# Performance work log

Measured on AMD Instinct MI355X. Metric: run time of the kernel, lower is better.

## Reference

```python
import jax, jax.numpy as jnp
import numpy as np

C = 768
NH = 8
S_SP = 9            # spatial size per axis; seq = 9**3 = 729
HID = (C * 4 * 2) // 3  # 2048, floor(768*8/3)
E = 3               # num_experts
TOPK = 2
EPS = 1e-5


def setup_inputs() -> dict:
    key = jax.random.key(0)
    ks = jax.random.split(key, 10)
    b = 8
    p = lambda k, shape: (jax.random.normal(k, shape, dtype=jnp.float32) * 0.02)
    return {
        "x": jax.random.normal(ks[0], (b, C, S_SP, S_SP, S_SP), dtype=jnp.float32),
        "ln_w": jnp.ones((C, S_SP, S_SP, S_SP), dtype=jnp.float32),
        "ln_b": jnp.zeros((C, S_SP, S_SP, S_SP), dtype=jnp.float32),
        "qkv_w": p(ks[1], (C, 3 * C)),
        "proj_w": p(ks[2], (C, C)),
        "router_w": p(ks[3], (C, E)),
        "gate_w": p(ks[4], (E, C, HID)),
        "up_w": p(ks[5], (E, C, HID)),
        "down_w": p(ks[6], (E, HID, C)),
    }


def _ablock(x, ln_w, ln_b, qkv_w, proj_w, router_w, gate_w, up_w, down_w):
    b, c, t, h, w = x.shape
    s = t * h * w
    dh = c // NH

    # LayerNorm over normalized_shape = (c, t, h, w)
    mean = jnp.mean(x, axis=(1, 2, 3, 4), keepdims=True)
    var = jnp.var(x, axis=(1, 2, 3, 4), keepdims=True)
    y = (x - mean) * jax.lax.rsqrt(var + EPS) * ln_w + ln_b

    # Attention (note: source applies NO 1/sqrt(dh) scaling)
    tok = jnp.transpose(y.reshape(b, c, s), (0, 2, 1))        # (b, s, c)
    qkv = (tok @ qkv_w).reshape(b, s, 3, NH, dh)
    qkv = jnp.transpose(qkv, (2, 0, 3, 1, 4))                  # (3, b, nh, s, dh)
    q, k, v = qkv[0], qkv[1], qkv[2]
    attn = jax.nn.softmax(jnp.einsum("bhsd,bhtd->bhst", q, k), axis=-1)
    o = jnp.einsum("bhst,bhtd->bhsd", attn, v)
    o = jnp.transpose(o, (0, 2, 1, 3)).reshape(b, s, c) @ proj_w  # (b, s, c)
    x = x + jnp.transpose(o, (0, 2, 1)).reshape(b, c, t, h, w)

    # MoE with top-2 routing over SwiGLU experts (dense compute)
    tok = jnp.transpose(x.reshape(b, c, s), (0, 2, 1))         # (b, s, c)
    probs = jax.nn.softmax(tok @ router_w, axis=-1)            # (b, s, E)
    vals, idx = jax.lax.top_k(probs, TOPK)
    vals = vals / jnp.sum(vals, axis=-1, keepdims=True)
    wfull = jnp.sum(jax.nn.one_hot(idx, E, dtype=tok.dtype) * vals[..., None], axis=2)  # (b, s, E)

    g = jnp.einsum("bsc,ech->bseh", tok, gate_w)
    u = jnp.einsum("bsc,ech->bseh", tok, up_w)
    hid = jax.nn.silu(g) * u                                   # (b, s, E, HID)
    eo = jnp.einsum("bseh,ehc->bsec", hid, down_w)             # (b, s, E, c)
    moe_out = jnp.einsum("bsec,bse->bsc", eo, wfull)

    return x + jnp.transpose(moe_out, (0, 2, 1)).reshape(b, c, t, h, w)


def reference(x, ln_w, ln_b, qkv_w, proj_w, router_w, gate_w, up_w, down_w):
    return _ablock(x, ln_w, ln_b, qkv_w, proj_w, router_w, gate_w, up_w, down_w)
```

## Files before the change

### kernel.cpp

```cpp
#include <hip/hip_runtime.h>
#include <hip/hip_bf16.h>

#define C_    768
#define NH_   8
#define DH_   96
#define S_    729
#define B_    8
#define MTOK  5832
#define C3    2304
#define GUN   12288
#define DK    6144
#define SPAD  736
#define NPB   559872

typedef __attribute__((ext_vector_type(8))) short short8;
typedef __attribute__((ext_vector_type(4))) float f32x4;
typedef __attribute__((ext_vector_type(4))) unsigned int uint4v;
typedef __hip_bfloat16 bf16;

__device__ __forceinline__ void gld_lds16(const bf16* g, bf16* l) {
  __builtin_amdgcn_global_load_lds((const __attribute__((address_space(1))) void*)g,
                                   (__attribute__((address_space(3))) void*)l, 16, 0, 0);
}
__device__ __forceinline__ void gld_lds16c(const char* g, char* l) {
  __builtin_amdgcn_global_load_lds((const __attribute__((address_space(1))) void*)g,
                                   (__attribute__((address_space(3))) void*)l, 16, 0, 0);
}

template<int DB>
__device__ __forceinline__ void tile_step(
    char* ldsc, char* ldsw,
    const int rA0, const int rA1, const int rB0, const int rB1,
    const char* pA0, const char* pA1, const char* pA2, const char* pA3,
    const char* pB0, const char* pB1, const char* pB2, const char* pB3,
    const int s1, const int s2, const bool gH1, const bool gH0, const int wmode,
    f32x4 (&acc)[8][4], short8 (&a4)[4][2], short8 (&b4)[4][2])
{
  const int DBO = DB * 65536;
  const int NBO = 65536 - DBO;
  #pragma unroll
  for (int mf = 0; mf < 4; ++mf) {
    a4[mf][0] = *(const short8*)(ldsc + DBO + rA0 + mf*2048);
    a4[mf][1] = *(const short8*)(ldsc + DBO + rA1 + mf*2048);
  }
  #pragma unroll
  for (int nf = 0; nf < 2; ++nf) {
    b4[nf][0] = *(const short8*)(ldsc + DBO + rB0 + nf*2048);
    b4[nf][1] = *(const short8*)(ldsc + DBO + rB1 + nf*2048);
  }
  if (gH1) {
    gld_lds16c(pA2 + s1, ldsw + NBO + 16384);
    gld_lds16c(pA3 + s1, ldsw + NBO + 16384 + 8192);
  }
  __builtin_amdgcn_s_barrier();
  asm volatile("s_waitcnt lgkmcnt(0)" ::: "memory");
  __builtin_amdgcn_sched_barrier(0);
  __builtin_amdgcn_s_setprio(1);
  #pragma unroll
  for (int mf = 0; mf < 4; ++mf)
    #pragma unroll
    for (int nf = 0; nf < 2; ++nf)
      #pragma unroll
      for (int j = 0; j < 2; ++j)
        acc[mf][nf] = __builtin_amdgcn_mfma_f32_16x16x32_bf16(a4[mf][j], b4[nf][j], acc[mf][nf], 0, 0, 0);
  __builtin_amdgcn_s_setprio(0);
  __builtin_amdgcn_s_barrier();
  #pragma unroll
  for (int nf = 2; nf < 4; ++nf) {
    b4[nf][0] = *(const short8*)(ldsc + DBO + rB0 + nf*2048);
    b4[nf][1] = *(const short8*)(ldsc + DBO + rB1 + nf*2048);
  }
  if (gH1) {
    gld_lds16c(pB2 + s1, ldsw + NBO + 32768 + 16384);
    gld_lds16c(pB3 + s1, ldsw + NBO + 32768 + 16384 + 8192);
  }
  __builtin_amdgcn_s_barrier();
  asm volatile("s_waitcnt lgkmcnt(0)" ::: "memory");
  __builtin_amdgcn_sched_barrier(0);
  __builtin_amdgcn_s_setprio(1);
  #pragma unroll
  for (int mf = 0; mf < 4; ++mf)
    #pragma unroll
    for (int nf = 2; nf < 4; ++nf)
      #pragma unroll
      for (int j = 0; j < 2; ++j)
        acc[mf][nf] = __builtin_amdgcn_mfma_f32_16x16x32_bf16(a4[mf][j], b4[nf][j], acc[mf][nf], 0, 0, 0);
  __builtin_amdgcn_s_setprio(0);
  __builtin_amdgcn_s_barrier();
  #pragma unroll
  for (int mi = 0; mi < 4; ++mi) {
    a4[mi][0] = *(const short8*)(ldsc + DBO + rA0 + (4+mi)*2048);
    a4[mi][1] = *(const short8*)(ldsc + DBO + rA1 + (4+mi)*2048);
  }
  if (gH0) {
    gld_lds16c(pB0 + s2, ldsw + DBO + 32768);
    gld_lds16c(pB1 + s2, ldsw + DBO + 32768 + 8192);
  }
  __builtin_amdgcn_s_barrier();
  asm volatile("s_waitcnt lgkmcnt(0)" ::: "memory");
  __builtin_amdgcn_sched_barrier(0);
  __builtin_amdgcn_s_setprio(1);
  #pragma unroll
  for (int mi = 0; mi < 4; ++mi)
    #pragma unroll
    for (int nf = 2; nf < 4; ++nf)
      #pragma unroll
      for (int j = 0; j < 2; ++j)
        acc[4+mi][nf] = __builtin_amdgcn_mfma_f32_16x16x32_bf16(a4[mi][j], b4[nf][j], acc[4+mi][nf], 0, 0, 0);
  __builtin_amdgcn_s_setprio(0);
  __builtin_amdgcn_s_barrier();
  if (gH0) {
    gld_lds16c(pA0 + s2, ldsw + DBO);
    gld_lds16c(pA1 + s2, ldsw + DBO + 8192);
  }
  __builtin_amdgcn_s_barrier();
  __builtin_amdgcn_s_setprio(1);
  #pragma unroll
  for (int mi = 0; mi < 4; ++mi)
    #pragma unroll
    for (int nf = 0; nf < 2; ++nf)
      #pragma unroll
      for (int j = 0; j < 2; ++j)
        acc[4+mi][nf] = __builtin_amdgcn_mfma_f32_16x16x32_bf16(a4[mi][j], b4[nf][j], acc[4+mi][nf], 0, 0, 0);
  __builtin_amdgcn_s_setprio(0);
  if (wmode == 0)      asm volatile("s_waitcnt vmcnt(4)" ::: "memory");
  else if (wmode == 1) asm volatile("s_waitcnt vmcnt(0)" ::: "memory");
  __builtin_amdgcn_s_barrier();
}

__global__ void __launch_bounds__(512, 2)
gemm8(const bf16* __restrict__ A, long a_rs,
      const bf16* __restrict__ Bt, long b_rs,
      float* __restrict__ Cf, bf16* __restrict__ Cb,
      long c_rs, long c_zoff, int M, int N, int Ksub)
{
  __shared__ __attribute__((aligned(128))) char ldsc[131072];
  const int tid = threadIdx.x;
  const int wid = tid >> 6, lid = tid & 63;
  const int wm = wid >> 2, wn = wid & 3;
  const int fr = lid & 15, g8 = (lid >> 4) * 8;
  const int brow = blockIdx.y * 256, bcol = blockIdx.x * 256;
  const long k0b = (long)blockIdx.z * Ksub * 2;
  const long a_rsb = a_rs * 2, b_rsb = b_rs * 2;
  const int srow = tid >> 3;
  const int scol = ((tid & 7) ^ (srow & 7)) << 4;
  const int NT = Ksub >> 6;
  char* ldsw = ldsc + wid * 1024;

  int ra0_ = brow + srow;        if (ra0_ > M-1) ra0_ = M-1;
  int ra1_ = brow + 64 + srow;   if (ra1_ > M-1) ra1_ = M-1;
  int ra2_ = brow + 128 + srow;  if (ra2_ > M-1) ra2_ = M-1;
  int ra3_ = brow + 192 + srow;  if (ra3_ > M-1) ra3_ = M-1;
  int rb0_ = bcol + srow;        if (rb0_ > N-1) rb0_ = N-1;
  int rb1_ = bcol + 64 + srow;   if (rb1_ > N-1) rb1_ = N-1;
  int rb2_ = bcol + 128 + srow;  if (rb2_ > N-1) rb2_ = N-1;
  int rb3_ = bcol + 192 + srow;  if (rb3_ > N-1) rb3_ = N-1;
  const char* pA0 = (const char*)A + (long)ra0_*a_rsb + k0b + scol;
  const char* pA1 = (const char*)A + (long)ra1_*a_rsb + k0b + scol;
  const char* pA2 = (const char*)A + (long)ra2_*a_rsb + k0b + scol;
  const char* pA3 = (const char*)A + (long)ra3_*a_rsb + k0b + scol;
  const char* pB0 = (const char*)Bt + (long)rb0_*b_rsb + k0b + scol;
  const char* pB1 = (const char*)Bt + (long)rb1_*b_rsb + k0b + scol;
  const char* pB2 = (const char*)Bt + (long)rb2_*b_rsb + k0b + scol;
  const char* pB3 = (const char*)Bt + (long)rb3_*b_rsb + k0b + scol;

  const int swz = (fr & 7) << 4;
  const int cx0 = (g8 * 2) ^ swz;
  const int cx1 = (64 + g8 * 2) ^ swz;
  const int rA0 = (wm*128 + fr)*128 + cx0;
  const int rA1 = (wm*128 + fr)*128 + cx1;
  const int rB0 = 32768 + (wn*64 + fr)*128 + cx0;
  const int rB1 = 32768 + (wn*64 + fr)*128 + cx1;

  f32x4 acc[8][4] = {};
  short8 a4[4][2], b4[4][2];

  gld_lds16c(pA0, ldsw);
  gld_lds16c(pA1, ldsw + 8192);
  gld_lds16c(pA2, ldsw + 16384);
  gld_lds16c(pA3, ldsw + 16384 + 8192);
  gld_lds16c(pB0, ldsw + 32768);
  gld_lds16c(pB1, ldsw + 32768 + 8192);
  gld_lds16c(pB2, ldsw + 32768 + 16384);
  gld_lds16c(pB3, ldsw + 32768 + 16384 + 8192);
  gld_lds16c(pA0 + 128, ldsw + 65536);
  gld_lds16c(pA1 + 128, ldsw + 65536 + 8192);
  gld_lds16c(pB0 + 128, ldsw + 65536 + 32768);
  gld_lds16c(pB1 + 128, ldsw + 65536 + 32768 + 8192);
  asm volatile("s_waitcnt vmcnt(4)" ::: "memory");
  __builtin_amdgcn_s_barrier();

  for (int tp = 0; tp < NT; tp += 2) {
    const bool g2 = (tp + 2) < NT;
    tile_step<0>(ldsc, ldsw, rA0, rA1, rB0, rB1,
                 pA0, pA1, pA2, pA3, pB0, pB1, pB2, pB3,
                 128, 256, true, g2, g2 ? 0 : 1, acc, a4, b4);
    tile_step<1>(ldsc, ldsw, rA0, rA1, rB0, rB1,
                 pA0, pA1, pA2, pA3, pB0, pB1, pB2, pB3,
                 256, 384, g2, g2, g2 ? 0 : 2, acc, a4, b4);
    if (g2) {
      pA0 += 256; pA1 += 256; pA2 += 256; pA3 += 256;
      pB0 += 256; pB1 += 256; pB2 += 256; pB3 += 256;
    }
  }

  const int rg = (lid >> 4) * 4;
  #pragma unroll
  for (int mf = 0; mf < 8; ++mf) {
    #pragma unroll
    for (int nf = 0; nf < 4; ++nf) {
      const int col = bcol + wn*64 + nf*16 + fr;
      if (col < N) {
        #pragma unroll
        for (int j = 0; j < 4; ++j) {
          const int row = brow + wm*128 + mf*16 + rg + j;
          if (row < M) {
            long off = (long)blockIdx.z*c_zoff + (long)row*c_rs + col;
            if (Cb) Cb[off] = __float2bfloat16(acc[mf][nf][j]);
            else    Cf[off] = acc[mf][nf][j];
          }
        }
      }
    }
  }
}

__global__ void __launch_bounds__(256)
gemm3_bt(const bf16* __restrict__ Ah, const bf16* __restrict__ Al,
         long a_rs, long a_oo, long a_oi,
         const bf16* __restrict__ Bth, const bf16* __restrict__ Btl,
         long b_rs, long b_oo, long b_oi,
         float* __restrict__ Cf, bf16* __restrict__ Ch, bf16* __restrict__ Cl,
         long c_rs, long c_oo, long c_oi,
         int M, int N, int K, int nlim, int zdiv)
{
  __shared__ bf16 lAh[4096];
  __shared__ bf16 lAl[4096];
  __shared__ bf16 lBh[4096];
  __shared__ bf16 lBl[4096];
  const int tid = threadIdx.x;
  const int wid = tid >> 6;
  const int lid = tid & 63;
  const int z = blockIdx.z;
  const int zo = z / zdiv, zi = z - zo*zdiv;
  const long aoff = (long)zo*a_oo + (long)zi*a_oi;
  const long boff = (long)zo*b_oo + (long)zi*b_oi;
  const long cbase = (long)zo*c_oo + (long)zi*c_oi;
  const int brow = blockIdx.y * 128;
  const int bcol = blockIdx.x * 128;

  const int ch0 = tid, ch1 = tid + 256;
  int ra0 = brow + (ch0 >> 2); if (ra0 > M-1) ra0 = M-1;
  int ra1 = brow + (ch1 >> 2); if (ra1 > M-1) ra1 = M-1;
  int rb0 = bcol + (ch0 >> 2); if (rb0 > N-1) rb0 = N-1;
  int rb1 = bcol + (ch1 >> 2); if (rb1 > N-1) rb1 = N-1;
  const int sw = ((ch0 ^ (ch0 >> 2)) & 3) * 8;
  const long ia0 = aoff + (long)ra0*a_rs + sw;
  const long ia1 = aoff + (long)ra1*a_rs + sw;
  const long ib0 = boff + (long)rb0*b_rs + sw;
  const long ib1 = boff + (long)rb1*b_rs + sw;
  bf16* dAh0 = (bf16*)((char*)lAh + wid*1024);
  bf16* dAh1 = (bf16*)((char*)lAh + 4096 + wid*1024);
  bf16* dAl0 = (bf16*)((char*)lAl + wid*1024);
  bf16* dAl1 = (bf16*)((char*)lAl + 4096 + wid*1024);
  bf16* dBh0 = (bf16*)((char*)lBh + wid*1024);
  bf16* dBh1 = (bf16*)((char*)lBh + 4096 + wid*1024);
  bf16* dBl0 = (bf16*)((char*)lBl + wid*1024);
  bf16* dBl1 = (bf16*)((char*)lBl + 4096 + wid*1024);

  f32x4 acc[4][4] = {};
  const int wm = wid >> 1, wn = wid & 1;
  const int fr = lid & 15, g8 = (lid >> 4) * 8;
  const int gx = g8 ^ ((lid & 3) << 3);

  for (int kt = 0; kt < K; kt += 32) {
    __syncthreads();
    gld_lds16(Ah + ia0 + kt, dAh0);
    gld_lds16(Ah + ia1 + kt, dAh1);
    gld_lds16(Al + ia0 + kt, dAl0);
    gld_lds16(Al + ia1 + kt, dAl1);
    gld_lds16(Bth + ib0 + kt, dBh0);
    gld_lds16(Bth + ib1 + kt, dBh1);
    gld_lds16(Btl + ib0 + kt, dBl0);
    gld_lds16(Btl + ib1 + kt, dBl1);
    __syncthreads();
    short8 fah[4], fal[4], fbh[4], fbl[4];
    #pragma unroll
    for (int m = 0; m < 4; ++m) {
      int ro = (wm*64 + m*16 + fr)*32 + gx;
      fah[m] = *(const short8*)&lAh[ro];
      fal[m] = *(const short8*)&lAl[ro];
    }
    #pragma unroll
    for (int n = 0; n < 4; ++n) {
      int ro = (wn*64 + n*16 + fr)*32 + gx;
      fbh[n] = *(const short8*)&lBh[ro];
      fbl[n] = *(const short8*)&lBl[ro];
    }
    #pragma unroll
    for (int m = 0; m < 4; ++m)
      #pragma unroll
      for (int n = 0; n < 4; ++n) {
        acc[m][n] = __builtin_amdgcn_mfma_f32_16x16x32_bf16(fal[m], fbh[n], acc[m][n], 0, 0, 0);
        acc[m][n] = __builtin_amdgcn_mfma_f32_16x16x32_bf16(fah[m], fbl[n], acc[m][n], 0, 0, 0);
        acc[m][n] = __builtin_amdgcn_mfma_f32_16x16x32_bf16(fah[m], fbh[n], acc[m][n], 0, 0, 0);
      }
  }

  const int rg = (lid >> 4) * 4;
  #pragma unroll
  for (int m = 0; m < 4; ++m) {
    #pragma unroll
    for (int n = 0; n < 4; ++n) {
      const int col = bcol + wn*64 + n*16 + fr;
      if (col < nlim) {
        #pragma unroll
        for (int j = 0; j < 4; ++j) {
          const int row = brow + wm*64 + m*16 + rg + j;
          if (row < M) {
            long off = cbase + (long)row*c_rs + col;
            float v = acc[m][n][j];
            if (Cl) {
              bf16 h = __float2bfloat16(v);
              Ch[off] = h;
              Cl[off] = __float2bfloat16(v - __bfloat162float(h));
            } else if (Ch) {
              Ch[off] = __float2bfloat16(v);
            } else {
              Cf[off] = v;
            }
          }
        }
      }
    }
  }
}

__global__ void wtrans(const float* __restrict__ in, bf16* __restrict__ out,
                       int R, int Cc, long in_rs, long out_rs, long in_bs, long out_bs)
{
  __shared__ float tile[32][33];
  in  += (long)blockIdx.z * in_bs;
  out += (long)blockIdx.z * out_bs;
  int r0 = blockIdx.y*32, c0 = blockIdx.x*32;
  int tx = threadIdx.x, ty = threadIdx.y;
  #pragma unroll
  for (int i = 0; i < 32; i += 8) {
    int r = r0 + ty + i, c = c0 + tx;
    if (r < R && c < Cc) tile[ty+i][tx] = in[(long)r*in_rs + c];
  }
  __syncthreads();
  #pragma unroll
  for (int i = 0; i < 32; i += 8) {
    int ro = c0 + ty + i, co = r0 + tx;
    if (ro < Cc && co < R) out[(long)ro*out_rs + co] = __float2bfloat16(tile[tx][ty+i]);
  }
}

__global__ void wtrans3(const float* __restrict__ in, bf16* __restrict__ oh, bf16* __restrict__ ol,
                        int R, int Cc, long in_rs, long out_rs)
{
  __shared__ float tile[32][33];
  int r0 = blockIdx.y*32, c0 = blockIdx.x*32;
  int tx = threadIdx.x, ty = threadIdx.y;
  #pragma unroll
  for (int i = 0; i < 32; i += 8) {
    int r = r0 + ty + i, c = c0 + tx;
    if (r < R && c < Cc) tile[ty+i][tx] = in[(long)r*in_rs + c];
  }
  __syncthreads();
  #pragma unroll
  for (int i = 0; i < 32; i += 8) {
    int ro = c0 + ty + i, co = r0 + tx;
    if (ro < Cc && co < R) {
      float v = tile[tx][ty+i];
      bf16 h = __float2bfloat16(v);
      long o = (long)ro*out_rs + co;
      oh[o] = h;
      ol[o] = __float2bfloat16(v - __bfloat162float(h));
    }
  }
}

__global__ void ln_partial(const float* __restrict__ x, float* __restrict__ part) {
  int b = blockIdx.y, blk = blockIdx.x;
  const float* xb = x + (long)b*NPB;
  int start = blk * 4374;
  float s = 0.f, ss = 0.f;
  for (int i = start + threadIdx.x; i < start + 4374; i += 256) {
    float v = xb[i]; s += v; ss += v*v;
  }
  #pragma unroll
  for (int o = 32; o; o >>= 1) { s += __shfl_down(s, o); ss += __shfl_down(ss, o); }
  __shared__ float red[2][4];
  int wid = threadIdx.x >> 6, lid = threadIdx.x & 63;
  if (lid == 0) { red[0][wid] = s; red[1][wid] = ss; }
  __syncthreads();
  if (threadIdx.x == 0) {
    float S = 0.f, SS = 0.f;
    for (int w = 0; w < 4; ++w) { S += red[0][w]; SS += red[1][w]; }
    part[(b*128 + blk)*2] = S; part[(b*128 + blk)*2 + 1] = SS;
  }
}

__global__ void ln_final(const float* __restrict__ part, float* __restrict__ stats) {
  int b = blockIdx.x, lid = threadIdx.x;
  float s = 0.f, ss = 0.f;
  for (int i = lid; i < 128; i += 64) { s += part[(b*128+i)*2]; ss += part[(b*128+i)*2+1]; }
  #pragma unroll
  for (int o = 32; o; o >>= 1) { s += __shfl_down(s, o); ss += __shfl_down(ss, o); }
  if (lid == 0) {
    float mean = s / (float)NPB;
    float var = ss / (float)NPB - mean*mean;
    stats[b*2] = mean; stats[b*2+1] = rsqrtf(var + 1e-5f);
  }
}

__global__ void ln_apply3(const float* __restrict__ x, const float* __restrict__ lnw,
                          const float* __restrict__ lnb, const float* __restrict__ stats,
                          bf16* __restrict__ th, bf16* __restrict__ tl)
{
  __shared__ float tile[32][33];
  int b = blockIdx.z;
  int s0 = blockIdx.x*32, c0 = blockIdx.y*32;
  float mean = stats[b*2], rstd = stats[b*2+1];
  int tx = threadIdx.x, ty = threadIdx.y;
  #pragma unroll
  for (int i = 0; i < 32; i += 8) {
    int c = c0 + ty + i, s = s0 + tx;
    if (s < S_) {
      long o = (long)c*S_ + s;
      tile[ty+i][tx] = (x[(long)b*NPB + o] - mean)*rstd*lnw[o] + lnb[o];
    }
  }
  __syncthreads();
  #pragma unroll
  for (int i = 0; i < 32; i += 8) {
    int s = s0 + ty + i, c = c0 + tx;
    if (s < S_) {
      float v = tile[tx][ty+i];
      bf16 h = __float2bfloat16(v);
      long o = ((long)b*S_ + s)*C_ + c;
      th[o] = h;
      tl[o] = __float2bfloat16(v - __bfloat162float(h));
    }
  }
}

__global__ void vtrans(const bf16* __restrict__ qkv, bf16* __restrict__ VT) {
  __shared__ float tile[32][33];
  int z = blockIdx.z; int bb = z >> 3, h = z & 7;
  const bf16* v = qkv + (long)bb*S_*C3 + 1536 + h*DH_;
  bf16* o = VT + (long)z*DH_*SPAD;
  int t0 = blockIdx.y*32, d0 = blockIdx.x*32;
  int tx = threadIdx.x, ty = threadIdx.y;
  #pragma unroll
  for (int i = 0; i < 32; i += 8) {
    int t = t0 + ty + i, d = d0 + tx;
    float val = 0.f;
    if (t < S_ && d < DH_) val = __bfloat162float(v[(long)t*C3 + d]);
    tile[ty+i][tx] = val;
  }
  __syncthreads();
  #pragma unroll
  for (int i = 0; i < 32; i += 8) {
    int d = d0 + ty + i, t = t0 + tx;
    if (d < DH_ && t < SPAD) o[(long)d*SPAD + t] = __float2bfloat16(tile[tx][ty+i]);
  }
}

__global__ void softmax3p(bf16* __restrict__ scores, int nrows) {
  int row = blockIdx.x*4 + (threadIdx.x >> 6);
  if (row >= nrows) return;
  int lid = threadIdx.x & 63;
  bf16* ph = scores + (long)row*2*SPAD;
  bf16* pl = ph + SPAD;
  float vals[12];
  float mx = -1e30f;
  #pragma unroll
  for (int i = 0; i < 12; ++i) {
    int t = i*64 + lid;
    float v = -1e30f;
    if (t < S_) v = __bfloat162float(ph[t]) + __bfloat162float(pl[t]);
    vals[i] = v; mx = fmaxf(mx, v);
  }
  #pragma unroll
  for (int o = 32; o; o >>= 1) mx = fmaxf(mx, __shfl_xor(mx, o));
  float sum = 0.f;
  #pragma unroll
  for (int i = 0; i < 12; ++i) { float e = __expf(vals[i] - mx); vals[i] = e; sum += e; }
  #pragma unroll
  for (int o = 32; o; o >>= 1) sum += __shfl_xor(sum, o);
  float inv = 1.f / sum;
  #pragma unroll
  for (int i = 0; i < 12; ++i) {
    int t = i*64 + lid;
    if (t < SPAD) {
      float p = (t < S_) ? vals[i]*inv : 0.f;
      bf16 h = __float2bfloat16(p);
      ph[t] = h;
      pl[t] = __float2bfloat16(p - __bfloat162float(h));
    }
  }
}

__global__ void tadd1(const float* __restrict__ x, const float* __restrict__ oproj,
                      float* __restrict__ xattn, bf16* __restrict__ tok2,
                      float* __restrict__ tok2f)
{
  __shared__ float t_o[32][33];
  __shared__ float t_x[32][33];
  int b = blockIdx.z;
  int s0 = blockIdx.x*32, c0 = blockIdx.y*32;
  int tx = threadIdx.x, ty = threadIdx.y;
  #pragma unroll
  for (int i = 0; i < 32; i += 8) {
    int s = s0 + ty + i;
    if (s < S_) t_o[ty+i][tx] = oproj[((long)b*S_ + s)*C_ + c0 + tx];
    int s2 = s0 + tx;
    if (s2 < S_) t_x[ty+i][tx] = x[(long)b*NPB + (long)(c0+ty+i)*S_ + s2];
  }
  __syncthreads();
  #pragma unroll
  for (int i = 0; i < 32; i += 8) {
    int s = s0 + tx, c = c0 + ty + i;
    if (s < S_) xattn[(long)b*NPB + (long)c*S_ + s] = t_x[ty+i][tx] + t_o[tx][ty+i];
    int s2 = s0 + ty + i, c2 = c0 + tx;
    if (s2 < S_) {
      float v = t_x[tx][ty+i] + t_o[ty+i][tx];
      long o = ((long)b*S_ + s2)*C_ + c2;
      tok2[o] = __float2bfloat16(v);
      tok2f[o] = v;
    }
  }
}

__global__ void tadd2(const float* __restrict__ xattn, const bf16* __restrict__ prt,
                      float* __restrict__ out)
{
  __shared__ float t_m[32][33];
  __shared__ float t_x[32][33];
  int b = blockIdx.z;
  int s0 = blockIdx.x*32, c0 = blockIdx.y*32;
  int tx = threadIdx.x, ty = threadIdx.y;
  #pragma unroll
  for (int i = 0; i < 32; i += 8) {
    int s = s0 + ty + i;
    if (s < S_) {
      const bf16* p = prt + ((long)b*S_ + s)*GUN + c0 + tx;
      float acc = 0.f;
      #pragma unroll
      for (int z = 0; z < 8; ++z) acc += __bfloat162float(p[z*768]);
      t_m[ty+i][tx] = acc;
    }
    int s2 = s0 + tx;
    if (s2 < S_) t_x[ty+i][tx] = xattn[(long)b*NPB + (long)(c0+ty+i)*S_ + s2];
  }
  __syncthreads();
  #pragma unroll
  for (int i = 0; i < 32; i += 8) {
    int s = s0 + tx, c = c0 + ty + i;
    if (s < S_) out[(long)b*NPB + (long)c*S_ + s] = t_x[ty+i][tx] + t_m[tx][ty+i];
  }
}

__global__ void router_k(const float* __restrict__ tok2f, const float* __restrict__ rw,
                         float* __restrict__ wfull)
{
  int t = blockIdx.x*4 + (threadIdx.x >> 6);
  if (t >= MTOK) return;
  int lid = threadIdx.x & 63;
  const float* tk = tok2f + (long)t*C_;
  float a0 = 0.f, a1 = 0.f, a2 = 0.f;
  for (int i = lid; i < C_; i += 64) {
    float v = tk[i];
    a0 += v*rw[i*3+0]; a1 += v*rw[i*3+1]; a2 += v*rw[i*3+2];
  }
  #pragma unroll
  for (int o = 32; o; o >>= 1) {
    a0 += __shfl_xor(a0, o); a1 += __shfl_xor(a1, o); a2 += __shfl_xor(a2, o);
  }
  if (lid == 0) {
    float m = fmaxf(a0, fmaxf(a1, a2));
    float e0 = __expf(a0-m), e1 = __expf(a1-m), e2 = __expf(a2-m);
    int emin = 0; float pm = e0;
    if (e1 <= pm) { pm = e1; emin = 1; }
    if (e2 <= pm) { pm = e2; emin = 2; }
    float rest = e0 + e1 + e2 - pm;
    wfull[t*3+0] = (emin == 0) ? 0.f : e0/rest;
    wfull[t*3+1] = (emin == 1) ? 0.f : e1/rest;
    wfull[t*3+2] = (emin == 2) ? 0.f : e2/rest;
  }
}

__global__ void silu_k(bf16* __restrict__ GU, const float* __restrict__ wfull) {
  long tid8 = (long)blockIdx.x*256 + threadIdx.x;
  long idx = tid8 * 8;
  int m = (int)(idx / DK);
  int j = (int)(idx - (long)m*DK);
  int e = j >> 11;
  float w = wfull[m*3 + e];
  bf16* gp = GU + (long)m*GUN + j;
  const bf16* up = gp + DK;
  union U8 { uint4v u; bf16 h[8]; };
  U8 g8, u8, o8;
  g8.u = *(const uint4v*)gp;
  u8.u = *(const uint4v*)up;
  #pragma unroll
  for (int i = 0; i < 8; ++i) {
    float g = __bfloat162float(g8.h[i]);
    float u = __bfloat162float(u8.h[i]);
    float sg = g / (1.f + __expf(-g));
    o8.h[i] = __float2bfloat16(sg * u * w);
  }
  *(uint4v*)gp = o8.u;
}

static inline void launch_gemm3(hipStream_t st,
    const bf16* Ah, const bf16* Al, long a_rs, long a_oo, long a_oi,
    const bf16* Bh, const bf16* Bl, long b_rs, long b_oo, long b_oi,
    float* Cf, bf16* Ch, bf16* Cl, long c_rs, long c_oo, long c_oi,
    int M, int N, int K, int nlim, int zdiv, int nz)
{
  dim3 g((N + 127)/128, (M + 127)/128, nz);
  gemm3_bt<<<g, 256, 0, st>>>(Ah, Al, a_rs, a_oo, a_oi, Bh, Bl, b_rs, b_oo, b_oi,
                              Cf, Ch, Cl, c_rs, c_oo, c_oi, M, N, K, nlim, zdiv);
}

extern "C" void kernel_launch(void* const* d_in, const int* in_sizes, int n_in,
                              void* d_out, int out_size, void* d_ws, size_t ws_size,
                              hipStream_t stream)
{
  const float* x      = (const float*)d_in[0];
  const float* ln_w   = (const float*)d_in[1];
  const float* ln_b   = (const float*)d_in[2];
  const float* qkv_w  = (const float*)d_in[3];
  const float* proj_w = (const float*)d_in[4];
  const float* rout_w = (const float*)d_in[5];
  const float* gate_w = (const float*)d_in[6];
  const float* up_w   = (const float*)d_in[7];
  const float* down_w = (const float*)d_in[8];
  float* out = (float*)d_out;

  char* ws = (char*)d_ws;
  size_t off = 0;
  auto alloc = [&](size_t bytes) { size_t r = off; off += (bytes + 255) & ~(size_t)255; return r; };

  size_t o_stats = alloc(8*2*4);
  size_t o_part  = alloc(8*128*2*4);
  size_t o_wfull = alloc((size_t)MTOK*3*4);
  size_t o_qkvTh = alloc((size_t)C3*C_*2);
  size_t o_qkvTl = alloc((size_t)C3*C_*2);
  size_t o_prjTh = alloc((size_t)C_*C_*2);
  size_t o_prjTl = alloc((size_t)C_*C_*2);
  size_t o_guT   = alloc((size_t)GUN*C_*2);
  size_t o_downT = alloc((size_t)C_*DK*2);
  size_t o_xattn = alloc((size_t)B_*NPB*4);
  size_t o_tok2  = alloc((size_t)MTOK*C_*2);
  size_t o_tok2f = alloc((size_t)MTOK*C_*4);
  size_t big0 = off;
  size_t o_qkvh  = alloc((size_t)MTOK*C3*2);
  size_t o_qkvl  = alloc((size_t)MTOK*C3*2);
  size_t o_VTh   = alloc((size_t)64*DH_*SPAD*2);
  size_t o_VTl   = alloc((size_t)64*DH_*SPAD*2);
  size_t o_aoh   = alloc((size_t)MTOK*C_*2);
  size_t o_aol   = alloc((size_t)MTOK*C_*2);
  size_t o_union = alloc((size_t)32*S_*SPAD*4);
  size_t endA = off;
  off = big0;
  size_t o_GU = alloc((size_t)MTOK*GUN*2);
  size_t endB = off;
  size_t needed = endA > endB ? endA : endB;
  if (ws_size < needed) return;

  float* stats  = (float*)(ws + o_stats);
  float* part   = (float*)(ws + o_part);
  float* wfull  = (float*)(ws + o_wfull);
  bf16*  qkvTh  = (bf16*)(ws + o_qkvTh);
  bf16*  qkvTl  = (bf16*)(ws + o_qkvTl);
  bf16*  prjTh  = (bf16*)(ws + o_prjTh);
  bf16*  prjTl  = (bf16*)(ws + o_prjTl);
  bf16*  guT    = (bf16*)(ws + o_guT);
  bf16*  downT  = (bf16*)(ws + o_downT);
  float* xattn  = (float*)(ws + o_xattn);
  bf16*  tok2   = (bf16*)(ws + o_tok2);
  float* tok2f  = (float*)(ws + o_tok2f);
  bf16*  qkvh   = (bf16*)(ws + o_qkvh);
  bf16*  qkvl   = (bf16*)(ws + o_qkvl);
  bf16*  VTh    = (bf16*)(ws + o_VTh);
  bf16*  VTl    = (bf16*)(ws + o_VTl);
  bf16*  aoh    = (bf16*)(ws + o_aoh);
  bf16*  aol    = (bf16*)(ws + o_aol);
  bf16*  tokh   = (bf16*)(ws + o_union);
  bf16*  tokl   = (bf16*)(ws + o_union + (size_t)MTOK*C_*2);
  bf16*  Pbase  = (bf16*)(ws + o_union);
  float* oproj  = (float*)(ws + o_union);
  bf16*  GU     = (bf16*)(ws + o_GU);

  dim3 b32(32, 8);

  wtrans3<<<dim3(72,24,1), b32, 0, stream>>>(qkv_w,  qkvTh, qkvTl, 768, 2304, 2304, 768);
  wtrans3<<<dim3(24,24,1), b32, 0, stream>>>(proj_w, prjTh, prjTl, 768, 768,  768,  768);
  wtrans<<<dim3(64,24,3), b32, 0, stream>>>(gate_w, guT, 768, 2048, 2048, 768,
                                            (long)768*2048, (long)2048*768);
  wtrans<<<dim3(64,24,3), b32, 0, stream>>>(up_w, guT + (size_t)DK*C_, 768, 2048, 2048, 768,
                                            (long)768*2048, (long)2048*768);
  wtrans<<<dim3(24,64,3), b32, 0, stream>>>(down_w, downT, 2048, 768, 768, 6144,
                                            (long)2048*768, 2048);

  ln_partial<<<dim3(128,8), 256, 0, stream>>>(x, part);
  ln_final<<<8, 64, 0, stream>>>(part, stats);
  ln_apply3<<<dim3(23,24,8), b32, 0, stream>>>(x, ln_w, ln_b, stats, tokh, tokl);

  launch_gemm3(stream, tokh, tokl, C_, 0, 0, qkvTh, qkvTl, C_, 0, 0,
               nullptr, qkvh, qkvl, C3, 0, 0, MTOK, C3, C_, C3, 1, 1);

  vtrans<<<dim3(3,23,64), b32, 0, stream>>>(qkvh, VTh);
  vtrans<<<dim3(3,23,64), b32, 0, stream>>>(qkvl, VTl);

  for (int c = 0; c < 2; ++c) {
    const long qoff = (long)(4*c)*S_*C3;
    launch_gemm3(stream,
        qkvh + qoff, qkvl + qoff, C3, (long)S_*C3, DH_,
        qkvh + qoff + 768, qkvl + qoff + 768, C3, (long)S_*C3, DH_,
        nullptr, Pbase, Pbase + SPAD, 2*SPAD, (long)8*S_*2*SPAD, (long)S_*2*SPAD,
        S_, S_, DH_, SPAD, 8, 32);
    softmax3p<<<5832, 256, 0, stream>>>(Pbase, 32*S_);
    launch_gemm3(stream,
        Pbase, Pbase + SPAD, 2*SPAD, (long)8*S_*2*SPAD, (long)S_*2*SPAD,
        VTh + (size_t)c*32*DH_*SPAD, VTl + (size_t)c*32*DH_*SPAD, SPAD,
        (long)8*DH_*SPAD, (long)DH_*SPAD,
        nullptr, aoh + (size_t)(4*c)*S_*C_, aol + (size_t)(4*c)*S_*C_,
        C_, (long)S_*C_, DH_,
        S_, DH_, SPAD, DH_, 8, 32);
  }

  launch_gemm3(stream, aoh, aol, C_, 0, 0, prjTh, prjTl, C_, 0, 0,
               oproj, nullptr, nullptr, C_, 0, 0, MTOK, C_, C_, C_, 1, 1);

  tadd1<<<dim3(23,24,8), b32, 0, stream>>>(x, oproj, xattn, tok2, tok2f);

  router_k<<<1458, 256, 0, stream>>>(tok2f, rout_w, wfull);

  gemm8<<<dim3(GUN/256, 23, 1), 512, 0, stream>>>(
      tok2, C_, guT, C_, nullptr, GU, GUN, 0, MTOK, GUN, C_);
  silu_k<<<MTOK*DK/2048, 256, 0, stream>>>(GU, wfull);
  gemm8<<<dim3(C_/256, 23, 8), 512, 0, stream>>>(
      GU, GUN, downT, DK, nullptr, GU + DK, GUN, 768, MTOK, C_, DK/8);

  tadd2<<<dim3(23,24,8), b32, 0, stream>>>(xattn, GU + DK, out);
}
```

Before: 786.0 us.

## Fuse SwiGLU and routing weight into gate/up GEMM epilogue via interleaved weights

Gate and up weight rows are interleaved in 16-row groups so each warp's accumulator tile holds matching gate and up columns. The gate/up GEMM epilogue then applies silu, multiplies by up and the routing weight, and writes only the hidden activations. This removes the separate silu kernel and the round trip of the full gate/up output through memory. The split-K partials of the down GEMM now go to a separate compact buffer, which changes the layout tadd2 reads.

```diff
diff --git a/kernel.cpp b/kernel.cpp
--- a/kernel.cpp
+++ b/kernel.cpp
@@ -132,7 +132,8 @@
 gemm8(const bf16* __restrict__ A, long a_rs,
       const bf16* __restrict__ Bt, long b_rs,
       float* __restrict__ Cf, bf16* __restrict__ Cb,
-      long c_rs, long c_zoff, int M, int N, int Ksub)
+      long c_rs, long c_zoff, int M, int N, int Ksub,
+      const float* __restrict__ wfull, int mode)
 {
   __shared__ __attribute__((aligned(128))) char ldsc[131072];
   const int tid = threadIdx.x;
@@ -205,19 +206,42 @@
   }
 
   const int rg = (lid >> 4) * 4;
-  #pragma unroll
-  for (int mf = 0; mf < 8; ++mf) {
-    #pragma unroll
-    for (int nf = 0; nf < 4; ++nf) {
-      const int col = bcol + wn*64 + nf*16 + fr;
-      if (col < N) {
+  if (mode == 3) {
+    #pragma unroll
+    for (int mf = 0; mf < 8; ++mf) {
+      #pragma unroll
+      for (int np = 0; np < 2; ++np) {
+        const int hb = (bcol + wn*64 + np*32) >> 5;
+        const int h = hb*16 + fr;
+        const int e = h >> 11;
         #pragma unroll
         for (int j = 0; j < 4; ++j) {
           const int row = brow + wm*128 + mf*16 + rg + j;
           if (row < M) {
-            long off = (long)blockIdx.z*c_zoff + (long)row*c_rs + col;
-            if (Cb) Cb[off] = __float2bfloat16(acc[mf][nf][j]);
-            else    Cf[off] = acc[mf][nf][j];
+            float g = acc[mf][2*np][j];
+            float u = acc[mf][2*np+1][j];
+            float w = wfull[row*3 + e];
+            float sg = g / (1.f + __expf(-g));
+            Cb[(long)row*c_rs + h] = __float2bfloat16(sg * u * w);
+          }
+        }
+      }
+    }
+  } else {
+    #pragma unroll
+    for (int mf = 0; mf < 8; ++mf) {
+      #pragma unroll
+      for (int nf = 0; nf < 4; ++nf) {
+        const int col = bcol + wn*64 + nf*16 + fr;
+        if (col < N) {
+          #pragma unroll
+          for (int j = 0; j < 4; ++j) {
+            const int row = brow + wm*128 + mf*16 + rg + j;
+            if (row < M) {
+              long off = (long)blockIdx.z*c_zoff + (long)row*c_rs + col;
+              if (mode == 0) Cb[off] = __float2bfloat16(acc[mf][nf][j]);
+              else           Cf[off] = acc[mf][nf][j];
+            }
           }
         }
       }
@@ -337,7 +361,8 @@
 }
 
 __global__ void wtrans(const float* __restrict__ in, bf16* __restrict__ out,
-                       int R, int Cc, long in_rs, long out_rs, long in_bs, long out_bs)
+                       int R, int Cc, long in_rs, long out_rs, long in_bs, long out_bs,
+                       int ilv, int radd)
 {
   __shared__ float tile[32][33];
   in  += (long)blockIdx.z * in_bs;
@@ -353,7 +378,10 @@
   #pragma unroll
   for (int i = 0; i < 32; i += 8) {
     int ro = c0 + ty + i, co = r0 + tx;
-    if (ro < Cc && co < R) out[(long)ro*out_rs + co] = __float2bfloat16(tile[tx][ty+i]);
+    if (ro < Cc && co < R) {
+      int rr = ilv ? (((ro >> 4) << 5) + (ro & 15) + radd) : ro;
+      out[(long)rr*out_rs + co] = __float2bfloat16(tile[tx][ty+i]);
+    }
   }
 }
 
@@ -418,7 +446,7 @@
 
 __global__ void ln_apply3(const float* __restrict__ x, const float* __restrict__ lnw,
                           const float* __restrict__ lnb, const float* __restrict__ stats,
-                          bf16* __restrict__ th, bf16* __restrict__ tl)
+                          bf16* __restrict__ th, bf16* __restrict__ tl, long ts)
 {
   __shared__ float tile[32][33];
   int b = blockIdx.z;
@@ -440,7 +468,7 @@
     if (s < S_) {
       float v = tile[tx][ty+i];
       bf16 h = __float2bfloat16(v);
-      long o = ((long)b*S_ + s)*C_ + c;
+      long o = ((long)b*S_ + s)*ts + c;
       th[o] = h;
       tl[o] = __float2bfloat16(v - __bfloat162float(h));
     }
@@ -547,10 +575,10 @@
   for (int i = 0; i < 32; i += 8) {
     int s = s0 + ty + i;
     if (s < S_) {
-      const bf16* p = prt + ((long)b*S_ + s)*GUN + c0 + tx;
+      const bf16* p = prt + ((long)b*S_ + s)*768 + c0 + tx;
       float acc = 0.f;
       #pragma unroll
-      for (int z = 0; z < 8; ++z) acc += __bfloat162float(p[z*768]);
+      for (int z = 0; z < 8; ++z) acc += __bfloat162float(p[(long)z*MTOK*768]);
       t_m[ty+i][tx] = acc;
     }
     int s2 = s0 + tx;
@@ -591,29 +619,6 @@
     wfull[t*3+1] = (emin == 1) ? 0.f : e1/rest;
     wfull[t*3+2] = (emin == 2) ? 0.f : e2/rest;
   }
-}
-
-__global__ void silu_k(bf16* __restrict__ GU, const float* __restrict__ wfull) {
-  long tid8 = (long)blockIdx.x*256 + threadIdx.x;
-  long idx = tid8 * 8;
-  int m = (int)(idx / DK);
-  int j = (int)(idx - (long)m*DK);
-  int e = j >> 11;
-  float w = wfull[m*3 + e];
-  bf16* gp = GU + (long)m*GUN + j;
-  const bf16* up = gp + DK;
-  union U8 { uint4v u; bf16 h[8]; };
-  U8 g8, u8, o8;
-  g8.u = *(const uint4v*)gp;
-  u8.u = *(const uint4v*)up;
-  #pragma unroll
-  for (int i = 0; i < 8; ++i) {
-    float g = __bfloat162float(g8.h[i]);
-    float u = __bfloat162float(u8.h[i]);
-    float sg = g / (1.f + __expf(-g));
-    o8.h[i] = __float2bfloat16(sg * u * w);
-  }
-  *(uint4v*)gp = o8.u;
 }
 
 static inline void launch_gemm3(hipStream_t st,
@@ -668,7 +673,8 @@
   size_t o_union = alloc((size_t)32*S_*SPAD*4);
   size_t endA = off;
   off = big0;
-  size_t o_GU = alloc((size_t)MTOK*GUN*2);
+  size_t o_hid = alloc((size_t)MTOK*DK*2);
+  size_t o_prt = alloc((size_t)8*MTOK*768*2);
   size_t endB = off;
   size_t needed = endA > endB ? endA : endB;
   if (ws_size < needed) return;
@@ -695,22 +701,23 @@
   bf16*  tokl   = (bf16*)(ws + o_union + (size_t)MTOK*C_*2);
   bf16*  Pbase  = (bf16*)(ws + o_union);
   float* oproj  = (float*)(ws + o_union);
-  bf16*  GU     = (bf16*)(ws + o_GU);
+  bf16*  hidden = (bf16*)(ws + o_hid);
+  bf16*  prt    = (bf16*)(ws + o_prt);
 
   dim3 b32(32, 8);
 
   wtrans3<<<dim3(72,24,1), b32, 0, stream>>>(qkv_w,  qkvTh, qkvTl, 768, 2304, 2304, 768);
   wtrans3<<<dim3(24,24,1), b32, 0, stream>>>(proj_w, prjTh, prjTl, 768, 768,  768,  768);
   wtrans<<<dim3(64,24,3), b32, 0, stream>>>(gate_w, guT, 768, 2048, 2048, 768,
-                                            (long)768*2048, (long)2048*768);
-  wtrans<<<dim3(64,24,3), b32, 0, stream>>>(up_w, guT + (size_t)DK*C_, 768, 2048, 2048, 768,
-                                            (long)768*2048, (long)2048*768);
+                                            (long)768*2048, (long)4096*768, 1, 0);
+  wtrans<<<dim3(64,24,3), b32, 0, stream>>>(up_w, guT, 768, 2048, 2048, 768,
+                                            (long)768*2048, (long)4096*768, 1, 16);
   wtrans<<<dim3(24,64,3), b32, 0, stream>>>(down_w, downT, 2048, 768, 768, 6144,
-                                            (long)2048*768, 2048);
+                                            (long)2048*768, 2048, 0, 0);
 
   ln_partial<<<dim3(128,8), 256, 0, stream>>>(x, part);
   ln_final<<<8, 64, 0, stream>>>(part, stats);
-  ln_apply3<<<dim3(23,24,8), b32, 0, stream>>>(x, ln_w, ln_b, stats, tokh, tokl);
+  ln_apply3<<<dim3(23,24,8), b32, 0, stream>>>(x, ln_w, ln_b, stats, tokh, tokl, C_);
 
   launch_gemm3(stream, tokh, tokl, C_, 0, 0, qkvTh, qkvTl, C_, 0, 0,
                nullptr, qkvh, qkvl, C3, 0, 0, MTOK, C3, C_, C3, 1, 1);
@@ -743,10 +750,11 @@
   router_k<<<1458, 256, 0, stream>>>(tok2f, rout_w, wfull);
 
   gemm8<<<dim3(GUN/256, 23, 1), 512, 0, stream>>>(
-      tok2, C_, guT, C_, nullptr, GU, GUN, 0, MTOK, GUN, C_);
-  silu_k<<<MTOK*DK/2048, 256, 0, stream>>>(GU, wfull);
+      tok2, C_, guT, C_, nullptr, hidden, DK, 0, MTOK, GUN, C_, wfull, 3);
+
   gemm8<<<dim3(C_/256, 23, 8), 512, 0, stream>>>(
-      GU, GUN, downT, DK, nullptr, GU + DK, GUN, 768, MTOK, C_, DK/8);
-
-  tadd2<<<dim3(23,24,8), b32, 0, stream>>>(xattn, GU + DK, out);
-}
+      hidden, DK, downT, DK, nullptr, prt, 768, (long)MTOK*768, MTOK, C_, DK/8,
+      nullptr, 0);
+
+  tadd2<<<dim3(23,24,8), b32, 0, stream>>>(xattn, prt, out);
+}
```

Measured after the change: 782.5 us. No clear change (-0.4%).
